# Kernel tuning notes

Hardware: AMD Instinct MI355X
Metric: run time of the kernel (lower is better)

Reference implementation:

```python
import jax, jax.numpy as jnp
import numpy as np

NEG_BIG = -9e15
ALPHA = 0.2  # LeakyReLU negative slope


def _gatm_layer(x, adj_mask, M, W, a_self, a_neighs):
    # x: [N, Fin], adj_mask: [N, N] bool, M: [N, N]
    h = x @ W                                   # [N, Fout]
    s = h @ a_self                              # [N, 1]
    n = h @ a_neighs                            # [N, 1]
    e = s + n.T                                 # [N, N] broadcast additive score
    e = jax.nn.leaky_relu(e * M, negative_slope=ALPHA)
    scores = jnp.where(adj_mask, e, NEG_BIG)
    attention = jax.nn.softmax(scores, axis=1)  # row-wise
    h_prime = attention @ h                     # [N, Fout]
    return jax.nn.elu(h_prime)                  # concat=True path


def setup_inputs() -> dict:
    key = jax.random.key(0)
    ks = jax.random.split(key, 8)
    N, D0, D1, D2 = 8192, 512, 256, 64
    scale = 0.05
    return {
        "x": jax.random.normal(ks[0], (N, D0), dtype=jnp.float32),
        "adj": jax.random.randint(ks[1], (N, N), 0, 2, dtype=jnp.int32),
        "M": jax.random.uniform(ks[2], (N, N), dtype=jnp.float32),
        "W0": jax.random.normal(ks[3], (D0, D1), dtype=jnp.float32) * scale,
        "a_self0": jax.random.normal(ks[4], (D1, 1), dtype=jnp.float32) * scale,
        "a_neighs0": jax.random.normal(ks[5], (D1, 1), dtype=jnp.float32) * scale,
        "W1": jax.random.normal(ks[6], (D1, D2), dtype=jnp.float32) * scale,
        "a_self1": jax.random.normal(ks[7], (D2, 1), dtype=jnp.float32) * scale,
        "a_neighs1": jax.random.normal(jax.random.fold_in(key, 99), (D2, 1), dtype=jnp.float32) * scale,
    }


def reference(x, adj, M, W0, a_self0, a_neighs0, W1, a_self1, a_neighs1):
    adj_mask = adj > 0
    x = _gatm_layer(x, adj_mask, M, W0, a_self0, a_neighs0)
    x = _gatm_layer(x, adj_mask, M, W1, a_self1, a_neighs1)
    return x
```

## Files before the change

### kernel.cpp

```cpp
#include <hip/hip_runtime.h>
#include <hip/hip_bf16.h>

constexpr int NN = 8192;
using uint = unsigned int;

typedef __bf16 bf16x8 __attribute__((ext_vector_type(8)));
typedef float f32x4 __attribute__((ext_vector_type(4)));
typedef float f32x16 __attribute__((ext_vector_type(16)));
typedef unsigned short ushort8_t __attribute__((ext_vector_type(8)));

__device__ __forceinline__ float eluf(float z) { return z > 0.f ? z : __expf(z) - 1.f; }

__device__ __forceinline__ unsigned short bf16_hi(float v) {
  unsigned u = __float_as_uint(v);
  unsigned r = u + 0x7fffu + ((u >> 16) & 1u);
  return (unsigned short)(r >> 16);
}
__device__ __forceinline__ float bf16_tof(unsigned short u) {
  return __uint_as_float(((unsigned)u) << 16);
}

__device__ __forceinline__ uint cvt_pk_bf16(float a, float b) {
  uint r;
  asm("v_cvt_pk_bf16_f32 %0, %1, %2" : "=v"(r) : "v"(a), "v"(b));
  return r;
}

__device__ __forceinline__ void lds_barrier() {
  asm volatile("s_waitcnt lgkmcnt(0)" ::: "memory");
  __builtin_amdgcn_s_barrier();
}

template<int K, int NOUT>
__global__ __launch_bounds__(256) void gemm_kernel(
    const float* __restrict__ A, const float* __restrict__ W, float* __restrict__ C) {
  constexpr int BM = 64, BN = 64, BK = 16;
  __shared__ __align__(16) float As[BK][BM + 4];
  __shared__ __align__(16) float Ws[BK][BN];
  const int t = threadIdx.x;
  const int i0 = blockIdx.x * BM;
  const int c0 = blockIdx.y * BN;
  const int tr = t >> 4;
  const int tc = t & 15;
  const int lr = t >> 2;
  const int lk = (t & 3) * 4;
  const int wk = t >> 4;
  const int wc = (t & 15) * 4;
  float acc[4][4] = {};
  for (int k0 = 0; k0 < K; k0 += BK) {
    const float4 a4 = *reinterpret_cast<const float4*>(&A[(size_t)(i0 + lr) * K + k0 + lk]);
    As[lk + 0][lr] = a4.x; As[lk + 1][lr] = a4.y;
    As[lk + 2][lr] = a4.z; As[lk + 3][lr] = a4.w;
    *reinterpret_cast<float4*>(&Ws[wk][wc]) =
        *reinterpret_cast<const float4*>(&W[(size_t)(k0 + wk) * NOUT + c0 + wc]);
    __syncthreads();
    #pragma unroll
    for (int kk = 0; kk < BK; ++kk) {
      const float4 av = *reinterpret_cast<const float4*>(&As[kk][4 * tr]);
      const float4 wv = *reinterpret_cast<const float4*>(&Ws[kk][4 * tc]);
      const float a[4] = {av.x, av.y, av.z, av.w};
      const float w[4] = {wv.x, wv.y, wv.z, wv.w};
      #pragma unroll
      for (int i = 0; i < 4; ++i)
        #pragma unroll
        for (int j = 0; j < 4; ++j) acc[i][j] += a[i] * w[j];
    }
    __syncthreads();
  }
  #pragma unroll
  for (int i = 0; i < 4; ++i) {
    const float4 o = make_float4(acc[i][0], acc[i][1], acc[i][2], acc[i][3]);
    *reinterpret_cast<float4*>(&C[(size_t)(i0 + 4 * tr + i) * NOUT + c0 + 4 * tc]) = o;
  }
}

template<int FOUT>
__global__ __launch_bounds__(256) void sn_kernel(
    const float* __restrict__ H, const float* __restrict__ a_self,
    const float* __restrict__ a_neigh, float* __restrict__ s, float* __restrict__ n) {
  const int wave = threadIdx.x >> 6;
  const int lane = threadIdx.x & 63;
  const int row = blockIdx.x * 4 + wave;
  float ds = 0.f, dn = 0.f;
  #pragma unroll
  for (int c = lane; c < FOUT; c += 64) {
    const float h = H[(size_t)row * FOUT + c];
    ds += h * a_self[c];
    dn += h * a_neigh[c];
  }
  #pragma unroll
  for (int off = 32; off > 0; off >>= 1) {
    ds += __shfl_down(ds, off);
    dn += __shfl_down(dn, off);
  }
  if (lane == 0) { s[row] = ds; n[row] = dn; }
}

template<int F>
__global__ __launch_bounds__(256) void split_kernel(
    const float* __restrict__ H, unsigned short* __restrict__ Th,
    unsigned short* __restrict__ Tl) {
  const int t = threadIdx.x;
  const int tile = blockIdx.x;
  const int c = t & (F - 1);
  const int kcb = t / F;
  for (int kc = kcb; kc < 4; kc += 256 / F) {
    ushort8_t hi, lo;
    #pragma unroll
    for (int e = 0; e < 8; ++e) {
      float v = H[(size_t)(tile * 32 + kc * 8 + e) * F + c];
      unsigned short h = bf16_hi(v);
      hi[e] = h;
      lo[e] = bf16_hi(v - bf16_tof(h));
    }
    size_t o = ((size_t)(tile * 4 + kc) * F + c) * 8;
    *reinterpret_cast<ushort8_t*>(&Th[o]) = hi;
    *reinterpret_cast<ushort8_t*>(&Tl[o]) = lo;
  }
}

__global__ __launch_bounds__(256) void mask_kernel(
    const int* __restrict__ adj, uint* __restrict__ Bm) {
  const size_t tg = (size_t)blockIdx.x * 256 + threadIdx.x;
  const int4 a = *reinterpret_cast<const int4*>(&adj[tg * 4]);
  uint nib = (a.x > 0 ? 1u : 0u) | (a.y > 0 ? 2u : 0u) |
             (a.z > 0 ? 4u : 0u) | (a.w > 0 ? 8u : 0u);
  const int lane = threadIdx.x & 63;
  uint v = nib << ((lane & 7) * 4);
  v |= __shfl_xor(v, 1);
  v |= __shfl_xor(v, 2);
  v |= __shfl_xor(v, 4);
  if ((lane & 7) == 0) Bm[tg >> 3] = v;
}

template<int F>
__global__ __launch_bounds__(256) void combine_kernel(
    const float* __restrict__ pO, const float* __restrict__ pL, float* __restrict__ out) {
  const size_t q = (size_t)blockIdx.x * 256 + threadIdx.x;
  const size_t base = q * 4;
  const int row = (int)(base / F);
  const float4 a = *reinterpret_cast<const float4*>(pO + base);
  const float4 b = *reinterpret_cast<const float4*>(pO + (size_t)8192 * F + base);
  const float il = 1.0f / (pL[row] + pL[8192 + row]);
  float4 o;
  o.x = eluf((a.x + b.x) * il);
  o.y = eluf((a.y + b.y) * il);
  o.z = eluf((a.z + b.z) * il);
  o.w = eluf((a.w + b.w) * il);
  *reinterpret_cast<float4*>(out + base) = o;
}

__global__ __launch_bounds__(1024, 4) void attn1_kernel(
    const float* __restrict__ Mm, const uint* __restrict__ Bm,
    const float* __restrict__ sv, const float* __restrict__ nv,
    const unsigned short* __restrict__ Th, const unsigned short* __restrict__ Tl,
    float* __restrict__ pO, float* __restrict__ pL) {
  constexpr int F = 256, NT = 4096 / 64;
  __shared__ __align__(16) uint Pa[2][2][2][8 * 132];
  __shared__ __align__(16) float nvs[8192];
  __shared__ float l_lds[64];

  const int t = threadIdx.x;
  const int lane = t & 63;
  const int w = t >> 6;
  const int cf = w & 7;
  const int ks = w >> 3;
  const int r = t >> 5;
  const int p2 = t & 31;
  const int i0 = blockIdx.x * 64;
  const int jh = blockIdx.y;
  const size_t jbase = (size_t)jh * 4096;
  const int jt = jh * 128;

  reinterpret_cast<float4*>(nvs)[t] = reinterpret_cast<const float4*>(nv + jbase)[t];

  const float svrA = sv[i0 + r];
  const float svrB = sv[i0 + 32 + r];
  const size_t mrowA = (size_t)(i0 + r) * NN + jbase;
  const size_t mrowB = mrowA + (size_t)32 * NN;
  const uint* mkrowA = Bm + (size_t)(i0 + r) * (NN / 32) + jh * 128;
  const uint* mkrowB = mkrowA + (size_t)32 * (NN / 32);
  const int col = cf * 32 + (lane & 31);
  const size_t bo0 = ((size_t)(lane >> 5) * F + col) * 8;
  const int pidx = (p2 >> 2) * 132 + r * 4 + (p2 & 3);
  const int aidx = (ks * 4 + (lane >> 5)) * 132 + (lane & 31) * 4;

  float2 MA_e = *reinterpret_cast<const float2*>(&Mm[mrowA + 2 * p2]);
  float2 MA_o = *reinterpret_cast<const float2*>(&Mm[mrowA + 64 + 2 * p2]);
  float2 MB_e = *reinterpret_cast<const float2*>(&Mm[mrowB + 2 * p2]);
  float2 MB_o = *reinterpret_cast<const float2*>(&Mm[mrowB + 64 + 2 * p2]);
  uint mkA_e = mkrowA[p2 >> 4];
  uint mkA_o = mkrowA[2 + (p2 >> 4)];
  uint mkB_e = mkrowB[p2 >> 4];
  uint mkB_o = mkrowB[2 + (p2 >> 4)];
  const size_t tb0 = (size_t)(jt + ks) * 8192;
  bf16x8 bh0_e = *reinterpret_cast<const bf16x8*>(Th + tb0 + bo0);
  bf16x8 bl0_e = *reinterpret_cast<const bf16x8*>(Tl + tb0 + bo0);
  bf16x8 bh1_e = *reinterpret_cast<const bf16x8*>(Th + tb0 + bo0 + 4096);
  bf16x8 bl1_e = *reinterpret_cast<const bf16x8*>(Tl + tb0 + bo0 + 4096);
  bf16x8 bh0_o, bl0_o, bh1_o, bl1_o;

  float rsumA = 0.f, rsumB = 0.f;
  f32x16 accA, accB;
  #pragma unroll
  for (int i = 0; i < 16; ++i) { accA[i] = 0.f; accB[i] = 0.f; }

  __syncthreads();

  float2 nv_e = *reinterpret_cast<const float2*>(&nvs[2 * p2]);
  float2 nv_o = *reinterpret_cast<const float2*>(&nvs[64 + 2 * p2]);

#define STEP1(TJ, MCA, MKA, MCB, MKB, NVC, BH0C, BL0C, BH1C, BL1C, BH0N, BL0N, BH1N, BL1N) \
  {                                                                               \
    const int t_j = (TJ);                                                         \
    const int jb = (t_j + 1 < NT) ? t_j + 1 : 0;                                  \
    const size_t tb = (size_t)(jt + 2 * jb + ks) * 8192;                          \
    BH0N = *reinterpret_cast<const bf16x8*>(Th + tb + bo0);                       \
    BL0N = *reinterpret_cast<const bf16x8*>(Tl + tb + bo0);                       \
    BH1N = *reinterpret_cast<const bf16x8*>(Th + tb + bo0 + 4096);                \
    BL1N = *reinterpret_cast<const bf16x8*>(Tl + tb + bo0 + 4096);                \
    float e0 = (svrA + NVC.x) * MCA.x; e0 = fmaxf(e0, 0.2f * e0); e0 = fminf(e0, 70.f); \
    float e1 = (svrA + NVC.y) * MCA.y; e1 = fmaxf(e1, 0.2f * e1); e1 = fminf(e1, 70.f); \
    float e2 = (svrB + NVC.x) * MCB.x; e2 = fmaxf(e2, 0.2f * e2); e2 = fminf(e2, 70.f); \
    float e3 = (svrB + NVC.y) * MCB.y; e3 = fmaxf(e3, 0.2f * e3); e3 = fminf(e3, 70.f); \
    const float pA0 = ((MKA >> (2 * (p2 & 15))) & 1u) ? __expf(e0) : 0.f;         \
    const float pA1 = ((MKA >> (2 * (p2 & 15) + 1)) & 1u) ? __expf(e1) : 0.f;     \
    const float pB0 = ((MKB >> (2 * (p2 & 15))) & 1u) ? __expf(e2) : 0.f;         \
    const float pB1 = ((MKB >> (2 * (p2 & 15) + 1)) & 1u) ? __expf(e3) : 0.f;     \
    rsumA += pA0 + pA1; rsumB += pB0 + pB1;                                       \
    const int jm = (t_j + 2 < NT) ? t_j + 2 : 0;                                  \
    MCA = *reinterpret_cast<const float2*>(&Mm[mrowA + (size_t)jm * 64 + 2 * p2]); \
    MKA = mkrowA[jm * 2 + (p2 >> 4)];                                             \
    MCB = *reinterpret_cast<const float2*>(&Mm[mrowB + (size_t)jm * 64 + 2 * p2]); \
    MKB = mkrowB[jm * 2 + (p2 >> 4)];                                             \
    NVC = *reinterpret_cast<const float2*>(&nvs[jm * 64 + 2 * p2]);               \
    const uint hwA = cvt_pk_bf16(pA0, pA1);                                       \
    const uint lwA = cvt_pk_bf16(pA0 - __uint_as_float(hwA << 16),                \
                                 pA1 - __uint_as_float(hwA & 0xffff0000u));       \
    const uint hwB = cvt_pk_bf16(pB0, pB1);                                       \
    const uint lwB = cvt_pk_bf16(pB0 - __uint_as_float(hwB << 16),                \
                                 pB1 - __uint_as_float(hwB & 0xffff0000u));       \
    Pa[t_j & 1][0][0][pidx] = hwA;                                                \
    Pa[t_j & 1][1][0][pidx] = lwA;                                                \
    Pa[t_j & 1][0][1][pidx] = hwB;                                                \
    Pa[t_j & 1][1][1][pidx] = lwB;                                                \
    lds_barrier();                                                                \
    const bf16x8 ahA0 = *reinterpret_cast<const bf16x8*>(&Pa[t_j & 1][0][0][aidx]);       \
    const bf16x8 alA0 = *reinterpret_cast<const bf16x8*>(&Pa[t_j & 1][1][0][aidx]);       \
    const bf16x8 ahA1 = *reinterpret_cast<const bf16x8*>(&Pa[t_j & 1][0][0][aidx + 264]); \
    const bf16x8 alA1 = *reinterpret_cast<const bf16x8*>(&Pa[t_j & 1][1][0][aidx + 264]); \
    const bf16x8 ahB0 = *reinterpret_cast<const bf16x8*>(&Pa[t_j & 1][0][1][aidx]);       \
    const bf16x8 alB0 = *reinterpret_cast<const bf16x8*>(&Pa[t_j & 1][1][1][aidx]);       \
    const bf16x8 ahB1 = *reinterpret_cast<const bf16x8*>(&Pa[t_j & 1][0][1][aidx + 264]); \
    const bf16x8 alB1 = *reinterpret_cast<const bf16x8*>(&Pa[t_j & 1][1][1][aidx + 264]); \
    accA = __builtin_amdgcn_mfma_f32_32x32x16_bf16(alA0, BH0C, accA, 0, 0, 0);    \
    accB = __builtin_amdgcn_mfma_f32_32x32x16_bf16(alB0, BH0C, accB, 0, 0, 0);    \
    accA = __builtin_amdgcn_mfma_f32_32x32x16_bf16(ahA0, BL0C, accA, 0, 0, 0);    \
    accB = __builtin_amdgcn_mfma_f32_32x32x16_bf16(ahB0, BL0C, accB, 0, 0, 0);    \
    accA = __builtin_amdgcn_mfma_f32_32x32x16_bf16(ahA0, BH0C, accA, 0, 0, 0);    \
    accB = __builtin_amdgcn_mfma_f32_32x32x16_bf16(ahB0, BH0C, accB, 0, 0, 0);    \
    accA = __builtin_amdgcn_mfma_f32_32x32x16_bf16(alA1, BH1C, accA, 0, 0, 0);    \
    accB = __builtin_amdgcn_mfma_f32_32x32x16_bf16(alB1, BH1C, accB, 0, 0, 0);    \
    accA = __builtin_amdgcn_mfma_f32_32x32x16_bf16(ahA1, BL1C, accA, 0, 0, 0);    \
    accB = __builtin_amdgcn_mfma_f32_32x32x16_bf16(ahB1, BL1C, accB, 0, 0, 0);    \
    accA = __builtin_amdgcn_mfma_f32_32x32x16_bf16(ahA1, BH1C, accA, 0, 0, 0);    \
    accB = __builtin_amdgcn_mfma_f32_32x32x16_bf16(ahB1, BH1C, accB, 0, 0, 0);    \
  }

  for (int tj = 0; tj < NT; tj += 2) {
    STEP1(tj,     MA_e, mkA_e, MB_e, mkB_e, nv_e, bh0_e, bl0_e, bh1_e, bl1_e, bh0_o, bl0_o, bh1_o, bl1_o)
    STEP1(tj + 1, MA_o, mkA_o, MB_o, mkB_o, nv_o, bh0_o, bl0_o, bh1_o, bl1_o, bh0_e, bl0_e, bh1_e, bl1_e)
  }
#undef STEP1

  #pragma unroll
  for (int off = 1; off < 32; off <<= 1) {
    rsumA += __shfl_xor(rsumA, off);
    rsumB += __shfl_xor(rsumB, off);
  }
  if (p2 == 0) { l_lds[r] = rsumA; l_lds[32 + r] = rsumB; }
  __syncthreads();
  if (t < 64) pL[(size_t)jh * 8192 + i0 + t] = l_lds[t];

  float* scratch = nvs;
  if (ks == 1) {
    #pragma unroll
    for (int reg = 0; reg < 16; ++reg) scratch[cf * 1024 + reg * 64 + lane] = accA[reg];
  }
  __syncthreads();
  if (ks == 0) {
    #pragma unroll
    for (int reg = 0; reg < 16; ++reg) {
      const int row = (reg & 3) + 8 * (reg >> 2) + 4 * (lane >> 5);
      pO[(size_t)jh * 8192 * F + (size_t)(i0 + row) * F + col] =
          accA[reg] + scratch[cf * 1024 + reg * 64 + lane];
    }
  }
  __syncthreads();
  if (ks == 1) {
    #pragma unroll
    for (int reg = 0; reg < 16; ++reg) scratch[cf * 1024 + reg * 64 + lane] = accB[reg];
  }
  __syncthreads();
  if (ks == 0) {
    #pragma unroll
    for (int reg = 0; reg < 16; ++reg) {
      const int row = (reg & 3) + 8 * (reg >> 2) + 4 * (lane >> 5);
      pO[(size_t)jh * 8192 * F + (size_t)(i0 + 32 + row) * F + col] =
          accB[reg] + scratch[cf * 1024 + reg * 64 + lane];
    }
  }
}

__global__ __launch_bounds__(1024, 4) void attn2_kernel(
    const float* __restrict__ Mm, const uint* __restrict__ Bm,
    const float* __restrict__ sv, const float* __restrict__ nv,
    const unsigned short* __restrict__ Th, const unsigned short* __restrict__ Tl,
    float* __restrict__ pO, float* __restrict__ pL) {
  constexpr int F = 64, NT = 4096 / 64;
  __shared__ __align__(16) uint Pa[2][2][2][8 * 132];
  __shared__ __align__(16) float nvs[4096];
  __shared__ float l_lds[64];

  const int t = threadIdx.x;
  const int lane = t & 63;
  const int w = t >> 6;
  const int rb = w & 1;
  const int cf = (w >> 1) & 3;
  const int ks = w >> 3;
  const int r = t >> 5;
  const int p2 = t & 31;
  const int i0 = blockIdx.x * 64;
  const int jh = blockIdx.y;
  const size_t jbase = (size_t)jh * 4096;
  const int jt = jh * 128;

  reinterpret_cast<float4*>(nvs)[t] = reinterpret_cast<const float4*>(nv + jbase)[t];

  const float svrA = sv[i0 + r];
  const float svrB = sv[i0 + 32 + r];
  const size_t mrowA = (size_t)(i0 + r) * NN + jbase;
  const size_t mrowB = mrowA + (size_t)32 * NN;
  const uint* mkrowA = Bm + (size_t)(i0 + r) * (NN / 32) + jh * 128;
  const uint* mkrowB = mkrowA + (size_t)32 * (NN / 32);
  const int col = cf * 16 + (lane & 15);
  const size_t bo2 = ((size_t)(lane >> 4) * F + col) * 8;
  const int pidx = (p2 >> 2) * 132 + r * 4 + (p2 & 3);
  const int aidx = (ks * 4 + (lane >> 4)) * 132 + (rb * 16 + (lane & 15)) * 4;

  float2 MA_e = *reinterpret_cast<const float2*>(&Mm[mrowA + 2 * p2]);
  float2 MA_o = *reinterpret_cast<const float2*>(&Mm[mrowA + 64 + 2 * p2]);
  float2 MB_e = *reinterpret_cast<const float2*>(&Mm[mrowB + 2 * p2]);
  float2 MB_o = *reinterpret_cast<const float2*>(&Mm[mrowB + 64 + 2 * p2]);
  uint mkA_e = mkrowA[p2 >> 4];
  uint mkA_o = mkrowA[2 + (p2 >> 4)];
  uint mkB_e = mkrowB[p2 >> 4];
  uint mkB_o = mkrowB[2 + (p2 >> 4)];
  const size_t tb0 = (size_t)(jt + ks) * 2048;
  bf16x8 bh_e = *reinterpret_cast<const bf16x8*>(Th + tb0 + bo2);
  bf16x8 bl_e = *reinterpret_cast<const bf16x8*>(Tl + tb0 + bo2);
  bf16x8 bh_o, bl_o;

  float rsumA = 0.f, rsumB = 0.f;
  f32x4 accA = {0.f, 0.f, 0.f, 0.f}, accA2 = {0.f, 0.f, 0.f, 0.f};
  f32x4 accB = {0.f, 0.f, 0.f, 0.f}, accB2 = {0.f, 0.f, 0.f, 0.f};

  __syncthreads();

  float2 nv_e = *reinterpret_cast<const float2*>(&nvs[2 * p2]);
  float2 nv_o = *reinterpret_cast<const float2*>(&nvs[64 + 2 * p2]);

#define STEP2(TJ, MCA, MKA, MCB, MKB, NVC, BHC, BLC, BHN, BLN)                    \
  {                                                                               \
    const int t_j = (TJ);                                                         \
    const int jb = (t_j + 1 < NT) ? t_j + 1 : 0;                                  \
    const size_t tb = (size_t)(jt + 2 * jb + ks) * 2048;                          \
    BHN = *reinterpret_cast<const bf16x8*>(Th + tb + bo2);                        \
    BLN = *reinterpret_cast<const bf16x8*>(Tl + tb + bo2);                        \
    float e0 = (svrA + NVC.x) * MCA.x; e0 = fmaxf(e0, 0.2f * e0); e0 = fminf(e0, 70.f); \
    float e1 = (svrA + NVC.y) * MCA.y; e1 = fmaxf(e1, 0.2f * e1); e1 = fminf(e1, 70.f); \
    float e2 = (svrB + NVC.x) * MCB.x; e2 = fmaxf(e2, 0.2f * e2); e2 = fminf(e2, 70.f); \
    float e3 = (svrB + NVC.y) * MCB.y; e3 = fmaxf(e3, 0.2f * e3); e3 = fminf(e3, 70.f); \
    const float pA0 = ((MKA >> (2 * (p2 & 15))) & 1u) ? __expf(e0) : 0.f;         \
    const float pA1 = ((MKA >> (2 * (p2 & 15) + 1)) & 1u) ? __expf(e1) : 0.f;     \
    const float pB0 = ((MKB >> (2 * (p2 & 15))) & 1u) ? __expf(e2) : 0.f;         \
    const float pB1 = ((MKB >> (2 * (p2 & 15) + 1)) & 1u) ? __expf(e3) : 0.f;     \
    rsumA += pA0 + pA1; rsumB += pB0 + pB1;                                       \
    const int jm = (t_j + 2 < NT) ? t_j + 2 : 0;                                  \
    MCA = *reinterpret_cast<const float2*>(&Mm[mrowA + (size_t)jm * 64 + 2 * p2]); \
    MKA = mkrowA[jm * 2 + (p2 >> 4)];                                             \
    MCB = *reinterpret_cast<const float2*>(&Mm[mrowB + (size_t)jm * 64 + 2 * p2]); \
    MKB = mkrowB[jm * 2 + (p2 >> 4)];                                             \
    NVC = *reinterpret_cast<const float2*>(&nvs[jm * 64 + 2 * p2]);               \
    const uint hwA = cvt_pk_bf16(pA0, pA1);                                       \
    const uint lwA = cvt_pk_bf16(pA0 - __uint_as_float(hwA << 16),                \
                                 pA1 - __uint_as_float(hwA & 0xffff0000u));       \
    const uint hwB = cvt_pk_bf16(pB0, pB1);                                       \
    const uint lwB = cvt_pk_bf16(pB0 - __uint_as_float(hwB << 16),                \
                                 pB1 - __uint_as_float(hwB & 0xffff0000u));       \
    Pa[t_j & 1][0][0][pidx] = hwA;                                                \
    Pa[t_j & 1][1][0][pidx] = lwA;                                                \
    Pa[t_j & 1][0][1][pidx] = hwB;                                                \
    Pa[t_j & 1][1][1][pidx] = lwB;                                                \
    lds_barrier();                                                                \
    const bf16x8 ahA = *reinterpret_cast<const bf16x8*>(&Pa[t_j & 1][0][0][aidx]); \
    const bf16x8 alA = *reinterpret_cast<const bf16x8*>(&Pa[t_j & 1][1][0][aidx]); \
    const bf16x8 ahB = *reinterpret_cast<const bf16x8*>(&Pa[t_j & 1][0][1][aidx]); \
    const bf16x8 alB = *reinterpret_cast<const bf16x8*>(&Pa[t_j & 1][1][1][aidx]); \
    accA  = __builtin_amdgcn_mfma_f32_16x16x32_bf16(alA, BHC, accA, 0, 0, 0);     \
    accB  = __builtin_amdgcn_mfma_f32_16x16x32_bf16(alB, BHC, accB, 0, 0, 0);     \
    accA2 = __builtin_amdgcn_mfma_f32_16x16x32_bf16(ahA, BLC, accA2, 0, 0, 0);    \
    accB2 = __builtin_amdgcn_mfma_f32_16x16x32_bf16(ahB, BLC, accB2, 0, 0, 0);    \
    accA  = __builtin_amdgcn_mfma_f32_16x16x32_bf16(ahA, BHC, accA, 0, 0, 0);     \
    accB  = __builtin_amdgcn_mfma_f32_16x16x32_bf16(ahB, BHC, accB, 0, 0, 0);     \
  }

  for (int tj = 0; tj < NT; tj += 2) {
    STEP2(tj,     MA_e, mkA_e, MB_e, mkB_e, nv_e, bh_e, bl_e, bh_o, bl_o)
    STEP2(tj + 1, MA_o, mkA_o, MB_o, mkB_o, nv_o, bh_o, bl_o, bh_e, bl_e)
  }
#undef STEP2

  #pragma unroll
  for (int off = 1; off < 32; off <<= 1) {
    rsumA += __shfl_xor(rsumA, off);
    rsumB += __shfl_xor(rsumB, off);
  }
  if (p2 == 0) { l_lds[r] = rsumA; l_lds[32 + r] = rsumB; }
  __syncthreads();
  if (t < 64) pL[(size_t)jh * 8192 + i0 + t] = l_lds[t];

  float* scratch = nvs;
  if (ks == 1) {
    #pragma unroll
    for (int reg = 0; reg < 4; ++reg)
      scratch[(w & 7) * 256 + reg * 64 + lane] = accA[reg] + accA2[reg];
  }
  __syncthreads();
  if (ks == 0) {
    #pragma unroll
    for (int reg = 0; reg < 4; ++reg) {
      const int row = rb * 16 + (lane >> 4) * 4 + reg;
      pO[(size_t)jh * 8192 * F + (size_t)(i0 + row) * F + col] =
          accA[reg] + accA2[reg] + scratch[(w & 7) * 256 + reg * 64 + lane];
    }
  }
  __syncthreads();
  if (ks == 1) {
    #pragma unroll
    for (int reg = 0; reg < 4; ++reg)
      scratch[(w & 7) * 256 + reg * 64 + lane] = accB[reg] + accB2[reg];
  }
  __syncthreads();
  if (ks == 0) {
    #pragma unroll
    for (int reg = 0; reg < 4; ++reg) {
      const int row = rb * 16 + (lane >> 4) * 4 + reg;
      pO[(size_t)jh * 8192 * F + (size_t)(i0 + 32 + row) * F + col] =
          accB[reg] + accB2[reg] + scratch[(w & 7) * 256 + reg * 64 + lane];
    }
  }
}

extern "C" void kernel_launch(void* const* d_in, const int* in_sizes, int n_in,
                              void* d_out, int out_size, void* d_ws, size_t ws_size,
                              hipStream_t stream) {
  const float* x   = (const float*)d_in[0];
  const int*   adj = (const int*)  d_in[1];
  const float* Mm  = (const float*)d_in[2];
  const float* W0  = (const float*)d_in[3];
  const float* as0 = (const float*)d_in[4];
  const float* an0 = (const float*)d_in[5];
  const float* W1  = (const float*)d_in[6];
  const float* as1 = (const float*)d_in[7];
  const float* an1 = (const float*)d_in[8];
  float* out = (float*)d_out;

  char* ws = (char*)d_ws;
  const size_t MB = 1048576;
  const size_t KB = 1024;
  float* h0  = (float*)(ws);
  uint*  Bm  = (uint*) (ws);
  float* x1  = (float*)(ws + 8 * MB);
  float* h1  = (float*)(ws + 16 * MB);
  unsigned short* Th0 = (unsigned short*)(ws + 18 * MB);
  unsigned short* Tl0 = (unsigned short*)(ws + 22 * MB);
  unsigned short* Th1 = (unsigned short*)(ws + 26 * MB);
  unsigned short* Tl1 = (unsigned short*)(ws + 27 * MB);
  float* s0  = (float*)(ws + 28 * MB);
  float* n0  = (float*)(ws + 28 * MB + 32 * KB);
  float* s1  = (float*)(ws + 28 * MB + 64 * KB);
  float* n1  = (float*)(ws + 28 * MB + 96 * KB);
  float* pL1 = (float*)(ws + 28 * MB + 128 * KB);
  float* pL2 = (float*)(ws + 28 * MB + 192 * KB);
  float* pO1 = (float*)(ws + 29 * MB);
  float* pO2 = (float*)(ws + 29 * MB);

  gemm_kernel<512, 256><<<dim3(128, 4), dim3(256), 0, stream>>>(x, W0, h0);
  sn_kernel<256><<<dim3(2048), dim3(256), 0, stream>>>(h0, as0, an0, s0, n0);
  split_kernel<256><<<dim3(256), dim3(256), 0, stream>>>(h0, Th0, Tl0);
  mask_kernel<<<dim3(65536), dim3(256), 0, stream>>>(adj, Bm);
  attn1_kernel<<<dim3(128, 2), dim3(1024), 0, stream>>>(Mm, Bm, s0, n0, Th0, Tl0, pO1, pL1);
  combine_kernel<256><<<dim3(2048), dim3(256), 0, stream>>>(pO1, pL1, x1);
  gemm_kernel<256, 64><<<dim3(128, 1), dim3(256), 0, stream>>>(x1, W1, h1);
  sn_kernel<64><<<dim3(2048), dim3(256), 0, stream>>>(h1, as1, an1, s1, n1);
  split_kernel<64><<<dim3(256), dim3(256), 0, stream>>>(h1, Th1, Tl1);
  attn2_kernel<<<dim3(128, 2), dim3(1024), 0, stream>>>(Mm, Bm, s1, n1, Th1, Tl1, pO2, pL2);
  combine_kernel<64><<<dim3(512), dim3(256), 0, stream>>>(pO2, pL2, out);
}
```

Baseline: 336.0 us.

## Retile layer-1 attention to 128-row blocks with 4-way column split and nontemporal loads

The layer-1 attention kernel now processes 128 rows per block over a quarter of the columns (grid 64x4), not 64 rows over half. Each loaded B tile of h is reused across twice as many rows, and the cross-wave LDS reduction of K-split partial accumulators is gone. A new combine kernel sums the four column-split partials. The M matrix, mask, and adj loads now use nontemporal hints to avoid polluting the cache. The costs are more partial-output traffic, higher register pressure, and no software prefetch of B tiles one step ahead.

```diff
diff --git a/kernel.cpp b/kernel.cpp
--- a/kernel.cpp
+++ b/kernel.cpp
@@ -24,6 +24,17 @@
   uint r;
   asm("v_cvt_pk_bf16_f32 %0, %1, %2" : "=v"(r) : "v"(a), "v"(b));
   return r;
+}
+
+__device__ __forceinline__ float2 ntload_f2(const float* p) {
+  const long long v = __builtin_nontemporal_load(reinterpret_cast<const long long*>(p));
+  float2 r;
+  r.x = __uint_as_float((uint)v);
+  r.y = __uint_as_float((uint)((unsigned long long)v >> 32));
+  return r;
+}
+__device__ __forceinline__ uint ntload_u32(const uint* p) {
+  return __builtin_nontemporal_load(p);
 }
 
 __device__ __forceinline__ void lds_barrier() {
@@ -122,15 +133,39 @@
 __global__ __launch_bounds__(256) void mask_kernel(
     const int* __restrict__ adj, uint* __restrict__ Bm) {
   const size_t tg = (size_t)blockIdx.x * 256 + threadIdx.x;
-  const int4 a = *reinterpret_cast<const int4*>(&adj[tg * 4]);
-  uint nib = (a.x > 0 ? 1u : 0u) | (a.y > 0 ? 2u : 0u) |
-             (a.z > 0 ? 4u : 0u) | (a.w > 0 ? 8u : 0u);
+  const long long* p = reinterpret_cast<const long long*>(adj) + tg * 2;
+  const long long v0 = __builtin_nontemporal_load(p);
+  const long long v1 = __builtin_nontemporal_load(p + 1);
+  const int a0 = (int)v0, a1 = (int)((unsigned long long)v0 >> 32);
+  const int a2 = (int)v1, a3 = (int)((unsigned long long)v1 >> 32);
+  uint nib = (a0 > 0 ? 1u : 0u) | (a1 > 0 ? 2u : 0u) |
+             (a2 > 0 ? 4u : 0u) | (a3 > 0 ? 8u : 0u);
   const int lane = threadIdx.x & 63;
   uint v = nib << ((lane & 7) * 4);
   v |= __shfl_xor(v, 1);
   v |= __shfl_xor(v, 2);
   v |= __shfl_xor(v, 4);
   if ((lane & 7) == 0) Bm[tg >> 3] = v;
+}
+
+template<int F>
+__global__ __launch_bounds__(256) void combine4_kernel(
+    const float* __restrict__ pO, const float* __restrict__ pL, float* __restrict__ out) {
+  const size_t q = (size_t)blockIdx.x * 256 + threadIdx.x;
+  const size_t base = q * 4;
+  const int row = (int)(base / F);
+  const size_t seg = (size_t)8192 * F;
+  const float4 a = *reinterpret_cast<const float4*>(pO + base);
+  const float4 b = *reinterpret_cast<const float4*>(pO + seg + base);
+  const float4 c = *reinterpret_cast<const float4*>(pO + 2 * seg + base);
+  const float4 d = *reinterpret_cast<const float4*>(pO + 3 * seg + base);
+  const float il = 1.0f / (pL[row] + pL[8192 + row] + pL[16384 + row] + pL[24576 + row]);
+  float4 o;
+  o.x = eluf((a.x + b.x + c.x + d.x) * il);
+  o.y = eluf((a.y + b.y + c.y + d.y) * il);
+  o.z = eluf((a.z + b.z + c.z + d.z) * il);
+  o.w = eluf((a.w + b.w + c.w + d.w) * il);
+  *reinterpret_cast<float4*>(out + base) = o;
 }
 
 template<int F>
@@ -150,165 +185,159 @@
   *reinterpret_cast<float4*>(out + base) = o;
 }
 
-__global__ __launch_bounds__(1024, 4) void attn1_kernel(
+__global__ __launch_bounds__(1024) void attn1_kernel(
     const float* __restrict__ Mm, const uint* __restrict__ Bm,
     const float* __restrict__ sv, const float* __restrict__ nv,
     const unsigned short* __restrict__ Th, const unsigned short* __restrict__ Tl,
     float* __restrict__ pO, float* __restrict__ pL) {
-  constexpr int F = 256, NT = 4096 / 64;
-  __shared__ __align__(16) uint Pa[2][2][2][8 * 132];
-  __shared__ __align__(16) float nvs[8192];
-  __shared__ float l_lds[64];
+  constexpr int F = 256, NT = 32;
+  __shared__ __align__(16) uint Pa[2][2][4][1056];
+  __shared__ __align__(16) float nvs[2048];
 
   const int t = threadIdx.x;
   const int lane = t & 63;
   const int w = t >> 6;
   const int cf = w & 7;
-  const int ks = w >> 3;
+  const int rgh = w >> 3;
   const int r = t >> 5;
   const int p2 = t & 31;
-  const int i0 = blockIdx.x * 64;
+  const int i0 = blockIdx.x * 128;
   const int jh = blockIdx.y;
-  const size_t jbase = (size_t)jh * 4096;
-  const int jt = jh * 128;
-
-  reinterpret_cast<float4*>(nvs)[t] = reinterpret_cast<const float4*>(nv + jbase)[t];
-
-  const float svrA = sv[i0 + r];
-  const float svrB = sv[i0 + 32 + r];
+  const size_t jbase = (size_t)jh * 2048;
+  const int jt32 = jh * 64;
+
+  reinterpret_cast<float2*>(nvs)[t] = reinterpret_cast<const float2*>(nv + jbase)[t];
+
+  const float svA = sv[i0 + r];
+  const float svB = sv[i0 + 32 + r];
+  const float svC = sv[i0 + 64 + r];
+  const float svD = sv[i0 + 96 + r];
   const size_t mrowA = (size_t)(i0 + r) * NN + jbase;
   const size_t mrowB = mrowA + (size_t)32 * NN;
-  const uint* mkrowA = Bm + (size_t)(i0 + r) * (NN / 32) + jh * 128;
-  const uint* mkrowB = mkrowA + (size_t)32 * (NN / 32);
+  const size_t mrowC = mrowA + (size_t)64 * NN;
+  const size_t mrowD = mrowA + (size_t)96 * NN;
+  const uint* mkA = Bm + (size_t)(i0 + r) * 256 + jh * 64;
+  const uint* mkB = mkA + 32 * 256;
+  const uint* mkC = mkA + 64 * 256;
+  const uint* mkD = mkA + 96 * 256;
   const int col = cf * 32 + (lane & 31);
-  const size_t bo0 = ((size_t)(lane >> 5) * F + col) * 8;
+  const size_t boA = ((size_t)(lane >> 5) * F + col) * 8;
   const int pidx = (p2 >> 2) * 132 + r * 4 + (p2 & 3);
-  const int aidx = (ks * 4 + (lane >> 5)) * 132 + (lane & 31) * 4;
-
-  float2 MA_e = *reinterpret_cast<const float2*>(&Mm[mrowA + 2 * p2]);
-  float2 MA_o = *reinterpret_cast<const float2*>(&Mm[mrowA + 64 + 2 * p2]);
-  float2 MB_e = *reinterpret_cast<const float2*>(&Mm[mrowB + 2 * p2]);
-  float2 MB_o = *reinterpret_cast<const float2*>(&Mm[mrowB + 64 + 2 * p2]);
-  uint mkA_e = mkrowA[p2 >> 4];
-  uint mkA_o = mkrowA[2 + (p2 >> 4)];
-  uint mkB_e = mkrowB[p2 >> 4];
-  uint mkB_o = mkrowB[2 + (p2 >> 4)];
-  const size_t tb0 = (size_t)(jt + ks) * 8192;
-  bf16x8 bh0_e = *reinterpret_cast<const bf16x8*>(Th + tb0 + bo0);
-  bf16x8 bl0_e = *reinterpret_cast<const bf16x8*>(Tl + tb0 + bo0);
-  bf16x8 bh1_e = *reinterpret_cast<const bf16x8*>(Th + tb0 + bo0 + 4096);
-  bf16x8 bl1_e = *reinterpret_cast<const bf16x8*>(Tl + tb0 + bo0 + 4096);
-  bf16x8 bh0_o, bl0_o, bh1_o, bl1_o;
-
-  float rsumA = 0.f, rsumB = 0.f;
-  f32x16 accA, accB;
-  #pragma unroll
-  for (int i = 0; i < 16; ++i) { accA[i] = 0.f; accB[i] = 0.f; }
+  const int aoff = (lane & 31) * 4;
+
+  float2 MA = ntload_f2(&Mm[mrowA + 2 * p2]);
+  float2 MB = ntload_f2(&Mm[mrowB + 2 * p2]);
+  float2 MC = ntload_f2(&Mm[mrowC + 2 * p2]);
+  float2 MD = ntload_f2(&Mm[mrowD + 2 * p2]);
+  uint KA = ntload_u32(&mkA[p2 >> 4]);
+  uint KB = ntload_u32(&mkB[p2 >> 4]);
+  uint KC = ntload_u32(&mkC[p2 >> 4]);
+  uint KD = ntload_u32(&mkD[p2 >> 4]);
+
+  float rsA = 0.f, rsB = 0.f, rsC = 0.f, rsD = 0.f;
+  f32x16 accP, accQ;
+  #pragma unroll
+  for (int i = 0; i < 16; ++i) { accP[i] = 0.f; accQ[i] = 0.f; }
 
   __syncthreads();
-
-  float2 nv_e = *reinterpret_cast<const float2*>(&nvs[2 * p2]);
-  float2 nv_o = *reinterpret_cast<const float2*>(&nvs[64 + 2 * p2]);
-
-#define STEP1(TJ, MCA, MKA, MCB, MKB, NVC, BH0C, BL0C, BH1C, BL1C, BH0N, BL0N, BH1N, BL1N) \
-  {                                                                               \
-    const int t_j = (TJ);                                                         \
-    const int jb = (t_j + 1 < NT) ? t_j + 1 : 0;                                  \
-    const size_t tb = (size_t)(jt + 2 * jb + ks) * 8192;                          \
-    BH0N = *reinterpret_cast<const bf16x8*>(Th + tb + bo0);                       \
-    BL0N = *reinterpret_cast<const bf16x8*>(Tl + tb + bo0);                       \
-    BH1N = *reinterpret_cast<const bf16x8*>(Th + tb + bo0 + 4096);                \
-    BL1N = *reinterpret_cast<const bf16x8*>(Tl + tb + bo0 + 4096);                \
-    float e0 = (svrA + NVC.x) * MCA.x; e0 = fmaxf(e0, 0.2f * e0); e0 = fminf(e0, 70.f); \
-    float e1 = (svrA + NVC.y) * MCA.y; e1 = fmaxf(e1, 0.2f * e1); e1 = fminf(e1, 70.f); \
-    float e2 = (svrB + NVC.x) * MCB.x; e2 = fmaxf(e2, 0.2f * e2); e2 = fminf(e2, 70.f); \
-    float e3 = (svrB + NVC.y) * MCB.y; e3 = fmaxf(e3, 0.2f * e3); e3 = fminf(e3, 70.f); \
-    const float pA0 = ((MKA >> (2 * (p2 & 15))) & 1u) ? __expf(e0) : 0.f;         \
-    const float pA1 = ((MKA >> (2 * (p2 & 15) + 1)) & 1u) ? __expf(e1) : 0.f;     \
-    const float pB0 = ((MKB >> (2 * (p2 & 15))) & 1u) ? __expf(e2) : 0.f;         \
-    const float pB1 = ((MKB >> (2 * (p2 & 15) + 1)) & 1u) ? __expf(e3) : 0.f;     \
-    rsumA += pA0 + pA1; rsumB += pB0 + pB1;                                       \
-    const int jm = (t_j + 2 < NT) ? t_j + 2 : 0;                                  \
-    MCA = *reinterpret_cast<const float2*>(&Mm[mrowA + (size_t)jm * 64 + 2 * p2]); \
-    MKA = mkrowA[jm * 2 + (p2 >> 4)];                                             \
-    MCB = *reinterpret_cast<const float2*>(&Mm[mrowB + (size_t)jm * 64 + 2 * p2]); \
-    MKB = mkrowB[jm * 2 + (p2 >> 4)];                                             \
-    NVC = *reinterpret_cast<const float2*>(&nvs[jm * 64 + 2 * p2]);               \
-    const uint hwA = cvt_pk_bf16(pA0, pA1);                                       \
-    const uint lwA = cvt_pk_bf16(pA0 - __uint_as_float(hwA << 16),                \
-                                 pA1 - __uint_as_float(hwA & 0xffff0000u));       \
-    const uint hwB = cvt_pk_bf16(pB0, pB1);                                       \
-    const uint lwB = cvt_pk_bf16(pB0 - __uint_as_float(hwB << 16),                \
-                                 pB1 - __uint_as_float(hwB & 0xffff0000u));       \
-    Pa[t_j & 1][0][0][pidx] = hwA;                                                \
-    Pa[t_j & 1][1][0][pidx] = lwA;                                                \
-    Pa[t_j & 1][0][1][pidx] = hwB;                                                \
-    Pa[t_j & 1][1][1][pidx] = lwB;                                                \
-    lds_barrier();                                                                \
-    const bf16x8 ahA0 = *reinterpret_cast<const bf16x8*>(&Pa[t_j & 1][0][0][aidx]);       \
-    const bf16x8 alA0 = *reinterpret_cast<const bf16x8*>(&Pa[t_j & 1][1][0][aidx]);       \
-    const bf16x8 ahA1 = *reinterpret_cast<const bf16x8*>(&Pa[t_j & 1][0][0][aidx + 264]); \
-    const bf16x8 alA1 = *reinterpret_cast<const bf16x8*>(&Pa[t_j & 1][1][0][aidx + 264]); \
-    const bf16x8 ahB0 = *reinterpret_cast<const bf16x8*>(&Pa[t_j & 1][0][1][aidx]);       \
-    const bf16x8 alB0 = *reinterpret_cast<const bf16x8*>(&Pa[t_j & 1][1][1][aidx]);       \
-    const bf16x8 ahB1 = *reinterpret_cast<const bf16x8*>(&Pa[t_j & 1][0][1][aidx + 264]); \
-    const bf16x8 alB1 = *reinterpret_cast<const bf16x8*>(&Pa[t_j & 1][1][1][aidx + 264]); \
-    accA = __builtin_amdgcn_mfma_f32_32x32x16_bf16(alA0, BH0C, accA, 0, 0, 0);    \
-    accB = __builtin_amdgcn_mfma_f32_32x32x16_bf16(alB0, BH0C, accB, 0, 0, 0);    \
-    accA = __builtin_amdgcn_mfma_f32_32x32x16_bf16(ahA0, BL0C, accA, 0, 0, 0);    \
-    accB = __builtin_amdgcn_mfma_f32_32x32x16_bf16(ahB0, BL0C, accB, 0, 0, 0);    \
-    accA = __builtin_amdgcn_mfma_f32_32x32x16_bf16(ahA0, BH0C, accA, 0, 0, 0);    \
-    accB = __builtin_amdgcn_mfma_f32_32x32x16_bf16(ahB0, BH0C, accB, 0, 0, 0);    \
-    accA = __builtin_amdgcn_mfma_f32_32x32x16_bf16(alA1, BH1C, accA, 0, 0, 0);    \
-    accB = __builtin_amdgcn_mfma_f32_32x32x16_bf16(alB1, BH1C, accB, 0, 0, 0);    \
-    accA = __builtin_amdgcn_mfma_f32_32x32x16_bf16(ahA1, BL1C, accA, 0, 0, 0);    \
-    accB = __builtin_amdgcn_mfma_f32_32x32x16_bf16(ahB1, BL1C, accB, 0, 0, 0);    \
-    accA = __builtin_amdgcn_mfma_f32_32x32x16_bf16(ahA1, BH1C, accA, 0, 0, 0);    \
-    accB = __builtin_amdgcn_mfma_f32_32x32x16_bf16(ahB1, BH1C, accB, 0, 0, 0);    \
-  }
-
-  for (int tj = 0; tj < NT; tj += 2) {
-    STEP1(tj,     MA_e, mkA_e, MB_e, mkB_e, nv_e, bh0_e, bl0_e, bh1_e, bl1_e, bh0_o, bl0_o, bh1_o, bl1_o)
-    STEP1(tj + 1, MA_o, mkA_o, MB_o, mkB_o, nv_o, bh0_o, bl0_o, bh1_o, bl1_o, bh0_e, bl0_e, bh1_e, bl1_e)
-  }
-#undef STEP1
+  float2 NV = *reinterpret_cast<const float2*>(&nvs[2 * p2]);
+
+  const int rg0 = rgh * 2, rg1 = rgh * 2 + 1;
+  const int mb = 2 * (p2 & 15);
+
+  #pragma unroll 2
+  for (int tj = 0; tj < NT; ++tj) {
+    const int buf = tj & 1;
+    bf16x8 bh[4], bl[4];
+    #pragma unroll
+    for (int s = 0; s < 4; ++s) {
+      const size_t ba = (size_t)(jt32 + 2 * tj + (s >> 1)) * 8192 + boA + (size_t)(s & 1) * 4096;
+      bh[s] = *reinterpret_cast<const bf16x8*>(Th + ba);
+      bl[s] = *reinterpret_cast<const bf16x8*>(Tl + ba);
+    }
+    float pA0, pA1, pB0, pB1, pC0, pC1, pD0, pD1;
+    {
+      float e0, e1;
+      e0 = (svA + NV.x) * MA.x; e0 = fmaxf(e0, 0.2f * e0); e0 = fminf(e0, 70.f);
+      e1 = (svA + NV.y) * MA.y; e1 = fmaxf(e1, 0.2f * e1); e1 = fminf(e1, 70.f);
+      pA0 = ((KA >> mb) & 1u) ? __expf(e0) : 0.f;
+      pA1 = ((KA >> (mb + 1)) & 1u) ? __expf(e1) : 0.f;
+      e0 = (svB + NV.x) * MB.x; e0 = fmaxf(e0, 0.2f * e0); e0 = fminf(e0, 70.f);
+      e1 = (svB + NV.y) * MB.y; e1 = fmaxf(e1, 0.2f * e1); e1 = fminf(e1, 70.f);
+      pB0 = ((KB >> mb) & 1u) ? __expf(e0) : 0.f;
+      pB1 = ((KB >> (mb + 1)) & 1u) ? __expf(e1) : 0.f;
+      e0 = (svC + NV.x) * MC.x; e0 = fmaxf(e0, 0.2f * e0); e0 = fminf(e0, 70.f);
+      e1 = (svC + NV.y) * MC.y; e1 = fmaxf(e1, 0.2f * e1); e1 = fminf(e1, 70.f);
+      pC0 = ((KC >> mb) & 1u) ? __expf(e0) : 0.f;
+      pC1 = ((KC >> (mb + 1)) & 1u) ? __expf(e1) : 0.f;
+      e0 = (svD + NV.x) * MD.x; e0 = fmaxf(e0, 0.2f * e0); e0 = fminf(e0, 70.f);
+      e1 = (svD + NV.y) * MD.y; e1 = fmaxf(e1, 0.2f * e1); e1 = fminf(e1, 70.f);
+      pD0 = ((KD >> mb) & 1u) ? __expf(e0) : 0.f;
+      pD1 = ((KD >> (mb + 1)) & 1u) ? __expf(e1) : 0.f;
+    }
+    rsA += pA0 + pA1; rsB += pB0 + pB1; rsC += pC0 + pC1; rsD += pD0 + pD1;
+    {
+      const int jm = (tj + 1 < NT) ? tj + 1 : 0;
+      MA = ntload_f2(&Mm[mrowA + (size_t)jm * 64 + 2 * p2]);
+      MB = ntload_f2(&Mm[mrowB + (size_t)jm * 64 + 2 * p2]);
+      MC = ntload_f2(&Mm[mrowC + (size_t)jm * 64 + 2 * p2]);
+      MD = ntload_f2(&Mm[mrowD + (size_t)jm * 64 + 2 * p2]);
+      KA = ntload_u32(&mkA[jm * 2 + (p2 >> 4)]);
+      KB = ntload_u32(&mkB[jm * 2 + (p2 >> 4)]);
+      KC = ntload_u32(&mkC[jm * 2 + (p2 >> 4)]);
+      KD = ntload_u32(&mkD[jm * 2 + (p2 >> 4)]);
+      NV = *reinterpret_cast<const float2*>(&nvs[jm * 64 + 2 * p2]);
+    }
+    {
+      uint hw, lw;
+      hw = cvt_pk_bf16(pA0, pA1);
+      lw = cvt_pk_bf16(pA0 - __uint_as_float(hw << 16), pA1 - __uint_as_float(hw & 0xffff0000u));
+      Pa[buf][0][0][pidx] = hw; Pa[buf][1][0][pidx] = lw;
+      hw = cvt_pk_bf16(pB0, pB1);
+      lw = cvt_pk_bf16(pB0 - __uint_as_float(hw << 16), pB1 - __uint_as_float(hw & 0xffff0000u));
+      Pa[buf][0][1][pidx] = hw; Pa[buf][1][1][pidx] = lw;
+      hw = cvt_pk_bf16(pC0, pC1);
+      lw = cvt_pk_bf16(pC0 - __uint_as_float(hw << 16), pC1 - __uint_as_float(hw & 0xffff0000u));
+      Pa[buf][0][2][pidx] = hw; Pa[buf][1][2][pidx] = lw;
+      hw = cvt_pk_bf16(pD0, pD1);
+      lw = cvt_pk_bf16(pD0 - __uint_as_float(hw << 16), pD1 - __uint_as_float(hw & 0xffff0000u));
+      Pa[buf][0][3][pidx] = hw; Pa[buf][1][3][pidx] = lw;
+    }
+    lds_barrier();
+    #pragma unroll
+    for (int s = 0; s < 4; ++s) {
+      const int ai = (2 * s + (lane >> 5)) * 132 + aoff;
+      const bf16x8 ah0 = *reinterpret_cast<const bf16x8*>(&Pa[buf][0][rg0][ai]);
+      const bf16x8 al0 = *reinterpret_cast<const bf16x8*>(&Pa[buf][1][rg0][ai]);
+      const bf16x8 ah1 = *reinterpret_cast<const bf16x8*>(&Pa[buf][0][rg1][ai]);
+      const bf16x8 al1 = *reinterpret_cast<const bf16x8*>(&Pa[buf][1][rg1][ai]);
+      accP = __builtin_amdgcn_mfma_f32_32x32x16_bf16(al0, bh[s], accP, 0, 0, 0);
+      accQ = __builtin_amdgcn_mfma_f32_32x32x16_bf16(al1, bh[s], accQ, 0, 0, 0);
+      accP = __builtin_amdgcn_mfma_f32_32x32x16_bf16(ah0, bl[s], accP, 0, 0, 0);
+      accQ = __builtin_amdgcn_mfma_f32_32x32x16_bf16(ah1, bl[s], accQ, 0, 0, 0);
+      accP = __builtin_amdgcn_mfma_f32_32x32x16_bf16(ah0, bh[s], accP, 0, 0, 0);
+      accQ = __builtin_amdgcn_mfma_f32_32x32x16_bf16(ah1, bh[s], accQ, 0, 0, 0);
+    }
+  }
 
   #pragma unroll
   for (int off = 1; off < 32; off <<= 1) {
-    rsumA += __shfl_xor(rsumA, off);
-    rsumB += __shfl_xor(rsumB, off);
-  }
-  if (p2 == 0) { l_lds[r] = rsumA; l_lds[32 + r] = rsumB; }
-  __syncthreads();
-  if (t < 64) pL[(size_t)jh * 8192 + i0 + t] = l_lds[t];
-
-  float* scratch = nvs;
-  if (ks == 1) {
-    #pragma unroll
-    for (int reg = 0; reg < 16; ++reg) scratch[cf * 1024 + reg * 64 + lane] = accA[reg];
-  }
-  __syncthreads();
-  if (ks == 0) {
-    #pragma unroll
-    for (int reg = 0; reg < 16; ++reg) {
-      const int row = (reg & 3) + 8 * (reg >> 2) + 4 * (lane >> 5);
-      pO[(size_t)jh * 8192 * F + (size_t)(i0 + row) * F + col] =
-          accA[reg] + scratch[cf * 1024 + reg * 64 + lane];
-    }
-  }
-  __syncthreads();
-  if (ks == 1) {
-    #pragma unroll
-    for (int reg = 0; reg < 16; ++reg) scratch[cf * 1024 + reg * 64 + lane] = accB[reg];
-  }
-  __syncthreads();
-  if (ks == 0) {
-    #pragma unroll
-    for (int reg = 0; reg < 16; ++reg) {
-      const int row = (reg & 3) + 8 * (reg >> 2) + 4 * (lane >> 5);
-      pO[(size_t)jh * 8192 * F + (size_t)(i0 + 32 + row) * F + col] =
-          accB[reg] + scratch[cf * 1024 + reg * 64 + lane];
-    }
+    rsA += __shfl_xor(rsA, off);
+    rsB += __shfl_xor(rsB, off);
+    rsC += __shfl_xor(rsC, off);
+    rsD += __shfl_xor(rsD, off);
+  }
+  if (p2 == 0) {
+    const size_t b = (size_t)jh * 8192 + i0 + r;
+    pL[b] = rsA; pL[b + 32] = rsB; pL[b + 64] = rsC; pL[b + 96] = rsD;
+  }
+
+  float* po = pO + (size_t)jh * 8192 * F;
+  #pragma unroll
+  for (int reg = 0; reg < 16; ++reg) {
+    const int rr = (reg & 3) + 8 * (reg >> 2) + 4 * (lane >> 5);
+    po[(size_t)(i0 + rgh * 64 + rr) * F + col] = accP[reg];
+    po[(size_t)(i0 + rgh * 64 + 32 + rr) * F + col] = accQ[reg];
   }
 }
 
@@ -348,14 +377,14 @@
   const int pidx = (p2 >> 2) * 132 + r * 4 + (p2 & 3);
   const int aidx = (ks * 4 + (lane >> 4)) * 132 + (rb * 16 + (lane & 15)) * 4;
 
-  float2 MA_e = *reinterpret_cast<const float2*>(&Mm[mrowA + 2 * p2]);
-  float2 MA_o = *reinterpret_cast<const float2*>(&Mm[mrowA + 64 + 2 * p2]);
-  float2 MB_e = *reinterpret_cast<const float2*>(&Mm[mrowB + 2 * p2]);
-  float2 MB_o = *reinterpret_cast<const float2*>(&Mm[mrowB + 64 + 2 * p2]);
-  uint mkA_e = mkrowA[p2 >> 4];
-  uint mkA_o = mkrowA[2 + (p2 >> 4)];
-  uint mkB_e = mkrowB[p2 >> 4];
-  uint mkB_o = mkrowB[2 + (p2 >> 4)];
+  float2 MA_e = ntload_f2(&Mm[mrowA + 2 * p2]);
+  float2 MA_o = ntload_f2(&Mm[mrowA + 64 + 2 * p2]);
+  float2 MB_e = ntload_f2(&Mm[mrowB + 2 * p2]);
+  float2 MB_o = ntload_f2(&Mm[mrowB + 64 + 2 * p2]);
+  uint mkA_e = ntload_u32(&mkrowA[p2 >> 4]);
+  uint mkA_o = ntload_u32(&mkrowA[2 + (p2 >> 4)]);
+  uint mkB_e = ntload_u32(&mkrowB[p2 >> 4]);
+  uint mkB_o = ntload_u32(&mkrowB[2 + (p2 >> 4)]);
   const size_t tb0 = (size_t)(jt + ks) * 2048;
   bf16x8 bh_e = *reinterpret_cast<const bf16x8*>(Th + tb0 + bo2);
   bf16x8 bl_e = *reinterpret_cast<const bf16x8*>(Tl + tb0 + bo2);
@@ -387,10 +416,10 @@
     const float pB1 = ((MKB >> (2 * (p2 & 15) + 1)) & 1u) ? __expf(e3) : 0.f;     \
     rsumA += pA0 + pA1; rsumB += pB0 + pB1;                                       \
     const int jm = (t_j + 2 < NT) ? t_j + 2 : 0;                                  \
-    MCA = *reinterpret_cast<const float2*>(&Mm[mrowA + (size_t)jm * 64 + 2 * p2]); \
-    MKA = mkrowA[jm * 2 + (p2 >> 4)];                                             \
-    MCB = *reinterpret_cast<const float2*>(&Mm[mrowB + (size_t)jm * 64 + 2 * p2]); \
-    MKB = mkrowB[jm * 2 + (p2 >> 4)];                                             \
+    MCA = ntload_f2(&Mm[mrowA + (size_t)jm * 64 + 2 * p2]);                       \
+    MKA = ntload_u32(&mkrowA[jm * 2 + (p2 >> 4)]);                                \
+    MCB = ntload_f2(&Mm[mrowB + (size_t)jm * 64 + 2 * p2]);                       \
+    MKB = ntload_u32(&mkrowB[jm * 2 + (p2 >> 4)]);                                \
     NVC = *reinterpret_cast<const float2*>(&nvs[jm * 64 + 2 * p2]);               \
     const uint hwA = cvt_pk_bf16(pA0, pA1);                                       \
     const uint lwA = cvt_pk_bf16(pA0 - __uint_as_float(hwA << 16),                \
@@ -492,7 +521,7 @@
   float* s1  = (float*)(ws + 28 * MB + 64 * KB);
   float* n1  = (float*)(ws + 28 * MB + 96 * KB);
   float* pL1 = (float*)(ws + 28 * MB + 128 * KB);
-  float* pL2 = (float*)(ws + 28 * MB + 192 * KB);
+  float* pL2 = (float*)(ws + 28 * MB + 256 * KB);
   float* pO1 = (float*)(ws + 29 * MB);
   float* pO2 = (float*)(ws + 29 * MB);
 
@@ -500,8 +529,8 @@
   sn_kernel<256><<<dim3(2048), dim3(256), 0, stream>>>(h0, as0, an0, s0, n0);
   split_kernel<256><<<dim3(256), dim3(256), 0, stream>>>(h0, Th0, Tl0);
   mask_kernel<<<dim3(65536), dim3(256), 0, stream>>>(adj, Bm);
-  attn1_kernel<<<dim3(128, 2), dim3(1024), 0, stream>>>(Mm, Bm, s0, n0, Th0, Tl0, pO1, pL1);
-  combine_kernel<256><<<dim3(2048), dim3(256), 0, stream>>>(pO1, pL1, x1);
+  attn1_kernel<<<dim3(64, 4), dim3(1024), 0, stream>>>(Mm, Bm, s0, n0, Th0, Tl0, pO1, pL1);
+  combine4_kernel<256><<<dim3(2048), dim3(256), 0, stream>>>(pO1, pL1, x1);
   gemm_kernel<256, 64><<<dim3(128, 1), dim3(256), 0, stream>>>(x1, W1, h1);
   sn_kernel<64><<<dim3(2048), dim3(256), 0, stream>>>(h1, as1, an1, s1, n1);
   split_kernel<64><<<dim3(256), dim3(256), 0, stream>>>(h1, Th1, Tl1);
```

Result: slower. 484.2 us (+44.1%).

## Run first projection GEMM on bf16 MFMA with hi/lo split for fp32 accuracy

Applied to the files above, without the earlier changes.

Replaces the fp32 FMA tiled GEMM for x@W0 with a matrix-core kernel that uses bf16 MFMA instructions. Inputs are pre-split into high and low bf16 parts in a K-blocked layout, and three MFMA products (hi*hi, hi*lo, lo*hi) approximate fp32 precision. This adds two preprocessing kernels and extra workspace traffic in exchange for much higher matrix throughput.

```diff
diff --git a/kernel.cpp b/kernel.cpp
--- a/kernel.cpp
+++ b/kernel.cpp
@@ -71,6 +71,89 @@
   for (int i = 0; i < 4; ++i) {
     const float4 o = make_float4(acc[i][0], acc[i][1], acc[i][2], acc[i][3]);
     *reinterpret_cast<float4*>(&C[(size_t)(i0 + 4 * tr + i) * NOUT + c0 + 4 * tc]) = o;
+  }
+}
+
+__global__ __launch_bounds__(256) void splitx_kernel(
+    const float* __restrict__ X, unsigned short* __restrict__ Th,
+    unsigned short* __restrict__ Tl) {
+  const size_t tid = (size_t)blockIdx.x * 256 + threadIdx.x;
+  const int kt = (int)(tid >> 13);
+  const int row = (int)(tid & 8191);
+  const float* src = X + (size_t)row * 512 + kt * 32;
+  #pragma unroll
+  for (int kc = 0; kc < 4; ++kc) {
+    ushort8_t hi, lo;
+    #pragma unroll
+    for (int e = 0; e < 8; ++e) {
+      const float v = src[kc * 8 + e];
+      const unsigned short h = bf16_hi(v);
+      hi[e] = h;
+      lo[e] = bf16_hi(v - bf16_tof(h));
+    }
+    const size_t o = ((size_t)(kt * 4 + kc) * 8192 + row) * 8;
+    *reinterpret_cast<ushort8_t*>(&Th[o]) = hi;
+    *reinterpret_cast<ushort8_t*>(&Tl[o]) = lo;
+  }
+}
+
+__global__ __launch_bounds__(256) void splitw_kernel(
+    const float* __restrict__ W, unsigned short* __restrict__ Th,
+    unsigned short* __restrict__ Tl) {
+  const int tid = blockIdx.x * 256 + threadIdx.x;
+  const int kb = tid >> 8;
+  const int col = tid & 255;
+  ushort8_t hi, lo;
+  #pragma unroll
+  for (int e = 0; e < 8; ++e) {
+    const float v = W[(size_t)(kb * 8 + e) * 256 + col];
+    const unsigned short h = bf16_hi(v);
+    hi[e] = h;
+    lo[e] = bf16_hi(v - bf16_tof(h));
+  }
+  const size_t o = ((size_t)kb * 256 + col) * 8;
+  *reinterpret_cast<ushort8_t*>(&Th[o]) = hi;
+  *reinterpret_cast<ushort8_t*>(&Tl[o]) = lo;
+}
+
+__global__ __launch_bounds__(512) void gemm1_mfma_kernel(
+    const unsigned short* __restrict__ Axh, const unsigned short* __restrict__ Axl,
+    const unsigned short* __restrict__ Bwh, const unsigned short* __restrict__ Bwl,
+    float* __restrict__ C) {
+  const int t = threadIdx.x;
+  const int lane = t & 63;
+  const int cf = t >> 6;
+  const int i0 = blockIdx.x * 32;
+  const int col = cf * 32 + (lane & 31);
+  const size_t abase = ((size_t)(lane >> 5) * 8192 + i0 + (lane & 31)) * 8;
+  const size_t bbase = ((size_t)(lane >> 5) * 256 + col) * 8;
+
+  f32x16 acc;
+  #pragma unroll
+  for (int i = 0; i < 16; ++i) acc[i] = 0.f;
+
+  #pragma unroll 2
+  for (int kt = 0; kt < 16; ++kt) {
+    const size_t at = (size_t)kt * 4 * 8192 * 8;
+    const size_t bt = (size_t)kt * 4 * 256 * 8;
+    #pragma unroll
+    for (int h = 0; h < 2; ++h) {
+      const size_t ao = at + (size_t)h * 2 * 8192 * 8 + abase;
+      const size_t bo = bt + (size_t)h * 2 * 256 * 8 + bbase;
+      const bf16x8 ah = *reinterpret_cast<const bf16x8*>(Axh + ao);
+      const bf16x8 al = *reinterpret_cast<const bf16x8*>(Axl + ao);
+      const bf16x8 bh = *reinterpret_cast<const bf16x8*>(Bwh + bo);
+      const bf16x8 bl = *reinterpret_cast<const bf16x8*>(Bwl + bo);
+      acc = __builtin_amdgcn_mfma_f32_32x32x16_bf16(al, bh, acc, 0, 0, 0);
+      acc = __builtin_amdgcn_mfma_f32_32x32x16_bf16(ah, bl, acc, 0, 0, 0);
+      acc = __builtin_amdgcn_mfma_f32_32x32x16_bf16(ah, bh, acc, 0, 0, 0);
+    }
+  }
+
+  #pragma unroll
+  for (int reg = 0; reg < 16; ++reg) {
+    const int row = (reg & 3) + 8 * (reg >> 2) + 4 * (lane >> 5);
+    C[(size_t)(i0 + row) * 256 + col] = acc[reg];
   }
 }
 
@@ -495,8 +578,14 @@
   float* pL2 = (float*)(ws + 28 * MB + 192 * KB);
   float* pO1 = (float*)(ws + 29 * MB);
   float* pO2 = (float*)(ws + 29 * MB);
-
-  gemm_kernel<512, 256><<<dim3(128, 4), dim3(256), 0, stream>>>(x, W0, h0);
+  unsigned short* Txh = (unsigned short*)(ws + 64 * MB);
+  unsigned short* Txl = (unsigned short*)(ws + 72 * MB);
+  unsigned short* Twh = (unsigned short*)(ws + 80 * MB);
+  unsigned short* Twl = (unsigned short*)(ws + 81 * MB);
+
+  splitx_kernel<<<dim3(512), dim3(256), 0, stream>>>(x, Txh, Txl);
+  splitw_kernel<<<dim3(64), dim3(256), 0, stream>>>(W0, Twh, Twl);
+  gemm1_mfma_kernel<<<dim3(256), dim3(512), 0, stream>>>(Txh, Txl, Twh, Twl, h0);
   sn_kernel<256><<<dim3(2048), dim3(256), 0, stream>>>(h0, as0, an0, s0, n0);
   split_kernel<256><<<dim3(256), dim3(256), 0, stream>>>(h0, Th0, Tl0);
   mask_kernel<<<dim3(65536), dim3(256), 0, stream>>>(adj, Bm);
```

After: 329.4 us. 1.02x faster.
